# Kernel optimization log

Hardware: AMD Instinct MI355X
Metric: run time of the kernel (lower is better)

## Reference

```python
import math
import jax, jax.numpy as jnp
import numpy as np

N_KV = 8
GROUP = 4
HEAD_DIM = 128
BATCH = 512
CACHE = 2048
CONTEXT = 4096
NEG_INF = -10000.0


def setup_inputs() -> dict:
    key = jax.random.key(0)
    k = jax.random.split(key, 6)
    queries = jax.random.normal(k[0], (N_KV * GROUP, BATCH, HEAD_DIM), jnp.float32)
    keys = jax.random.normal(k[1], (N_KV, BATCH, HEAD_DIM), jnp.float32)
    key_t_caches = jax.random.normal(k[2], (N_KV, HEAD_DIM, CACHE), jnp.float32)
    values = jax.random.normal(k[3], (N_KV, BATCH, HEAD_DIM), jnp.float32)
    value_caches = jax.random.normal(k[4], (N_KV, CACHE, HEAD_DIM), jnp.float32)
    # causal bias: token b (global position CACHE+b) may attend to positions <= CACHE+b;
    # padded tail [CACHE+BATCH, CONTEXT) is always masked with NEG_INF
    pos = jnp.arange(CONTEXT)[None, :]                       # [1, CONTEXT]
    limit = (CACHE + jnp.arange(BATCH))[:, None]             # [BATCH, 1]
    attn_bias = jnp.where(pos <= limit, 0.0, NEG_INF).astype(jnp.float32)
    kq_scale = jnp.asarray([1.0 / math.sqrt(HEAD_DIM)], jnp.float32)
    return {
        "queries": queries,
        "keys": keys,
        "key_t_caches": key_t_caches,
        "values": values,
        "value_caches": value_caches,
        "attn_bias": attn_bias,
        "kq_scale": kq_scale,
    }


def reference(queries, keys, key_t_caches, values, value_caches, attn_bias, kq_scale):
    n_kv, B, D = keys.shape
    n_heads = queries.shape[0]
    group = n_heads // n_kv
    cache = key_t_caches.shape[-1]
    context = attn_bias.shape[-1]
    pad = context - cache - B

    scaled_keys = keys * kq_scale                            # [kv, B, D]
    scaled_values = jnp.maximum(values, NEG_INF)             # [kv, B, D]

    # pad new keys/values to fill context, then prepend cache (matches torch pad+cat)
    padded_kt = jnp.pad(scaled_keys.transpose(0, 2, 1), ((0, 0), (0, 0), (0, pad)))
    all_keys_t = jnp.concatenate([key_t_caches, padded_kt], axis=-1)   # [kv, D, context]
    padded_v = jnp.pad(scaled_values, ((0, 0), (0, pad), (0, 0)))
    all_values = jnp.concatenate([value_caches, padded_v], axis=1)     # [kv, context, D]

    q = queries.reshape(n_kv, group, B, D)                   # group-major per kv head
    scores = jnp.einsum('kgbd,kdc->kgbc', q, all_keys_t) + attn_bias   # [kv, g, B, context]
    probs = jax.nn.softmax(scores, axis=-1)
    out = jnp.einsum('kgbc,kcd->kgbd', probs, all_values)    # [kv, g, B, D]
    head_outs = out.reshape(n_heads, B, D)
    return head_outs, scaled_keys, scaled_values
```

## Files before the change

### kernel.cpp

```cpp
#include <hip/hip_runtime.h>
#include <hip/hip_bf16.h>

#define NKV 8
#define NHEADS 32
#define HDIM 128
#define BATCH 512
#define CACHE 2048
#define CTX_TOT 2560
#define CT 64
#define KPITCH 136
#define VPITCH 72
#define PPITCH 72
#define NEG_BIG (-1e30f)

typedef __attribute__((ext_vector_type(8))) _Float16 half8;
typedef __attribute__((ext_vector_type(4))) float floatx4;


__global__ void kprep(const float* __restrict__ ktc, _Float16* __restrict__ Kh) {
    __shared__ float tile[32][33];
    int kv = blockIdx.z, c0 = blockIdx.x * 32, d0 = blockIdx.y * 32;
    int x = threadIdx.x, y = threadIdx.y;
    const float* src = ktc + ((size_t)kv * HDIM + d0) * CACHE + c0;
#pragma unroll
    for (int i = 0; i < 4; i++)
        tile[y + 8 * i][x] = src[(size_t)(y + 8 * i) * CACHE + x];
    __syncthreads();
    _Float16* dst = Kh + ((size_t)kv * CTX_TOT + c0) * HDIM + d0;
#pragma unroll
    for (int i = 0; i < 4; i++)
        dst[(size_t)(y + 8 * i) * HDIM + x] = (_Float16)tile[x][y + 8 * i];
}

__global__ void vprep(const float* __restrict__ vc, _Float16* __restrict__ Vth) {
    __shared__ float tile[32][33];
    int kv = blockIdx.z, c0 = blockIdx.x * 32, d0 = blockIdx.y * 32;
    int x = threadIdx.x, y = threadIdx.y;
    const float* src = vc + ((size_t)kv * CACHE + c0) * HDIM + d0;
#pragma unroll
    for (int i = 0; i < 4; i++)
        tile[y + 8 * i][x] = src[(size_t)(y + 8 * i) * HDIM + x];
    __syncthreads();
    _Float16* dst = Vth + ((size_t)kv * HDIM + d0) * CTX_TOT + c0;
#pragma unroll
    for (int i = 0; i < 4; i++)
        dst[(size_t)(y + 8 * i) * CTX_TOT + x] = (_Float16)tile[x][y + 8 * i];
}

__global__ void knew(const float* __restrict__ keys, const float* __restrict__ kq,
                     float* __restrict__ outk, _Float16* __restrict__ Kh) {
    int i = blockIdx.x * 256 + threadIdx.x;
    float s = kq[0];
    float v = keys[i] * s;
    outk[i] = v;
    int kv = i >> 16;
    int rem = i & 0xFFFF;
    Kh[((size_t)kv * CTX_TOT + CACHE) * HDIM + rem] = (_Float16)v;
}

__global__ void vnew(const float* __restrict__ values, float* __restrict__ outv,
                     _Float16* __restrict__ Vth) {
    __shared__ float tile[32][33];
    int kv = blockIdx.z, b0 = blockIdx.x * 32, d0 = blockIdx.y * 32;
    int x = threadIdx.x, y = threadIdx.y;
    const float* src = values + ((size_t)kv * BATCH + b0) * HDIM + d0;
    float* dst32 = outv + ((size_t)kv * BATCH + b0) * HDIM + d0;
#pragma unroll
    for (int i = 0; i < 4; i++) {
        float v = fmaxf(src[(size_t)(y + 8 * i) * HDIM + x], -10000.0f);
        tile[y + 8 * i][x] = v;
        dst32[(size_t)(y + 8 * i) * HDIM + x] = v;
    }
    __syncthreads();
    _Float16* dst = Vth + ((size_t)kv * HDIM + d0) * CTX_TOT + CACHE + b0;
#pragma unroll
    for (int i = 0; i < 4; i++)
        dst[(size_t)(y + 8 * i) * CTX_TOT + x] = (_Float16)tile[x][y + 8 * i];
}

__global__ __launch_bounds__(256) void attn_main(const float* __restrict__ q_g,
                                                 const _Float16* __restrict__ Kh,
                                                 const _Float16* __restrict__ Vth,
                                                 float* __restrict__ out) {
    __shared__ _Float16 Klds[CT * KPITCH];
    __shared__ _Float16 Vlds[HDIM * VPITCH];
    __shared__ _Float16 Plds[4][16 * PPITCH];

    const int h = blockIdx.x & 31;
    const int qb = blockIdx.x >> 5;
    const int kv = h >> 2;
    const int t = threadIdx.x;
    const int wave = t >> 6;
    const int lane = t & 63;
    const int l15 = lane & 15, quad = lane >> 4;

    const float LOG2E = 1.44269504088896340736f;
    const int qrow0 = qb * 64 + wave * 16;
    const float* qp = q_g + ((size_t)h * BATCH + qrow0 + l15) * HDIM + quad * 8;
    half8 qfrag[4];
#pragma unroll
    for (int kb = 0; kb < 4; kb++) {
        const float* p = qp + kb * 32;
        float4 a = *(const float4*)p;
        float4 b = *(const float4*)(p + 4);
        qfrag[kb][0] = (_Float16)(a.x * LOG2E); qfrag[kb][1] = (_Float16)(a.y * LOG2E);
        qfrag[kb][2] = (_Float16)(a.z * LOG2E); qfrag[kb][3] = (_Float16)(a.w * LOG2E);
        qfrag[kb][4] = (_Float16)(b.x * LOG2E); qfrag[kb][5] = (_Float16)(b.y * LOG2E);
        qfrag[kb][6] = (_Float16)(b.z * LOG2E); qfrag[kb][7] = (_Float16)(b.w * LOG2E);
    }

    floatx4 O[8];
#pragma unroll
    for (int nb = 0; nb < 8; nb++) O[nb] = (floatx4){0.f, 0.f, 0.f, 0.f};
    float m_r[4], l_r[4];
#pragma unroll
    for (int r = 0; r < 4; r++) { m_r[r] = NEG_BIG; l_r[r] = 0.f; }

    const int lim_wave = CACHE + qrow0 + 15;
    const int nT = 33 + qb;

    for (int tt = 0; tt < nT; tt++) {
        const int c0 = tt * CT;
        __syncthreads();
#pragma unroll
        for (int i = 0; i < 4; i++) {
            int ch = t + 256 * i;
            int row = ch >> 4, j = ch & 15;
            uint4 v = *(const uint4*)(Kh + ((size_t)kv * CTX_TOT + c0 + row) * HDIM + j * 8);
            *(uint4*)(&Klds[row * KPITCH + j * 8]) = v;
        }
#pragma unroll
        for (int i = 0; i < 4; i++) {
            int ch = t + 256 * i;
            int row = ch >> 3, j = ch & 7;
            uint4 v = *(const uint4*)(Vth + ((size_t)kv * HDIM + row) * CTX_TOT + c0 + j * 8);
            *(uint4*)(&Vlds[row * VPITCH + j * 8]) = v;
        }
        __syncthreads();

        if (c0 <= lim_wave) {
            floatx4 S[4];
#pragma unroll
            for (int cs = 0; cs < 4; cs++) {
                floatx4 acc = (floatx4){0.f, 0.f, 0.f, 0.f};
                int crow = cs * 16 + l15;
#pragma unroll
                for (int kb = 0; kb < 4; kb++) {
                    half8 kf = *(const half8*)(&Klds[crow * KPITCH + kb * 32 + quad * 8]);
                    acc = __builtin_amdgcn_mfma_f32_16x16x32_f16(qfrag[kb], kf, acc, 0, 0, 0);
                }
                S[cs] = acc;
            }
            if (c0 + CT > CACHE + qb * 64) {
#pragma unroll
                for (int cs = 0; cs < 4; cs++)
#pragma unroll
                    for (int r = 0; r < 4; r++) {
                        int c = c0 + cs * 16 + l15;
                        int brow = qrow0 + quad * 4 + r;
                        if (c > CACHE + brow) S[cs][r] = NEG_BIG;
                    }
            }
            float tmax[4];
#pragma unroll
            for (int r = 0; r < 4; r++)
                tmax[r] = fmaxf(fmaxf(S[0][r], S[1][r]), fmaxf(S[2][r], S[3][r]));
#pragma unroll
            for (int off = 8; off >= 1; off >>= 1)
#pragma unroll
                for (int r = 0; r < 4; r++)
                    tmax[r] = fmaxf(tmax[r], __shfl_xor(tmax[r], off, 64));
            float alpha[4];
#pragma unroll
            for (int r = 0; r < 4; r++) {
                float mn = fmaxf(m_r[r], tmax[r]);
                alpha[r] = __builtin_amdgcn_exp2f(m_r[r] - mn);
                m_r[r] = mn;
                l_r[r] *= alpha[r];
            }
#pragma unroll
            for (int nb = 0; nb < 8; nb++)
#pragma unroll
                for (int r = 0; r < 4; r++) O[nb][r] *= alpha[r];
#pragma unroll
            for (int cs = 0; cs < 4; cs++)
#pragma unroll
                for (int r = 0; r < 4; r++) {
                    float p = __builtin_amdgcn_exp2f(S[cs][r] - m_r[r]);
                    l_r[r] += p;
                    Plds[wave][(quad * 4 + r) * PPITCH + cs * 16 + l15] = (_Float16)p;
                }
#pragma unroll
            for (int kb2 = 0; kb2 < 2; kb2++) {
                half8 pf = *(const half8*)(&Plds[wave][l15 * PPITCH + kb2 * 32 + quad * 8]);
#pragma unroll
                for (int nb = 0; nb < 8; nb++) {
                    half8 vf = *(const half8*)(&Vlds[(nb * 16 + l15) * VPITCH + kb2 * 32 + quad * 8]);
                    O[nb] = __builtin_amdgcn_mfma_f32_16x16x32_f16(pf, vf, O[nb], 0, 0, 0);
                }
            }
        }
    }

#pragma unroll
    for (int off = 8; off >= 1; off >>= 1)
#pragma unroll
        for (int r = 0; r < 4; r++) l_r[r] += __shfl_xor(l_r[r], off, 64);
    float inv[4];
#pragma unroll
    for (int r = 0; r < 4; r++) inv[r] = 1.0f / l_r[r];
#pragma unroll
    for (int nb = 0; nb < 8; nb++)
#pragma unroll
        for (int r = 0; r < 4; r++) {
            int brow = qrow0 + quad * 4 + r;
            out[((size_t)h * BATCH + brow) * HDIM + nb * 16 + l15] = O[nb][r] * inv[r];
        }
}

extern "C" void kernel_launch(void* const* d_in, const int* in_sizes, int n_in,
                              void* d_out, int out_size, void* d_ws, size_t ws_size,
                              hipStream_t stream) {
    const float* queries = (const float*)d_in[0];
    const float* keys    = (const float*)d_in[1];
    const float* ktc     = (const float*)d_in[2];
    const float* values  = (const float*)d_in[3];
    const float* vcache  = (const float*)d_in[4];
    const float* kq      = (const float*)d_in[6];

    float* out     = (float*)d_out;
    float* out_sk  = out + (size_t)NHEADS * BATCH * HDIM;
    float* out_sv  = out_sk + (size_t)NKV * BATCH * HDIM;

    _Float16* Kh  = (_Float16*)d_ws;
    _Float16* Vth = Kh + (size_t)NKV * CTX_TOT * HDIM;

    kprep<<<dim3(64, 4, 8), dim3(32, 8), 0, stream>>>(ktc, Kh);
    vprep<<<dim3(64, 4, 8), dim3(32, 8), 0, stream>>>(vcache, Vth);
    knew<<<dim3(2048), dim3(256), 0, stream>>>(keys, kq, out_sk, Kh);
    vnew<<<dim3(16, 4, 8), dim3(32, 8), 0, stream>>>(values, out_sv, Vth);
    attn_main<<<dim3(256), dim3(256), 0, stream>>>(queries, Kh, Vth, out);
}
```

Before: 177.9 us.

## Split attention context across blocks with merge kernel and fuse prep kernels

Merges the four preprocessing kernels into one launch that dispatches on block index. It also splits each head/query-block's context loop four ways (interleaved tiles) across a second grid dimension, so there are 1024 blocks instead of 256. Each split writes unnormalized partial outputs plus its running max and sum, and a new merge kernel combines them with exp2 reweighting. This is meant to fix the low occupancy of only 256 blocks on a large GPU and cut launch overhead. The cost is extra workspace traffic for the partial results and one more kernel launch.

```diff
diff --git a/kernel.cpp b/kernel.cpp
--- a/kernel.cpp
+++ b/kernel.cpp
@@ -8,6 +8,7 @@
 #define CACHE 2048
 #define CTX_TOT 2560
 #define CT 64
+#define SPLITS 4
 #define KPITCH 136
 #define VPITCH 72
 #define PPITCH 72
@@ -16,78 +17,83 @@
 typedef __attribute__((ext_vector_type(8))) _Float16 half8;
 typedef __attribute__((ext_vector_type(4))) float floatx4;
 
-
-__global__ void kprep(const float* __restrict__ ktc, _Float16* __restrict__ Kh) {
+__global__ __launch_bounds__(256) void prep(const float* __restrict__ ktc,
+                                            const float* __restrict__ vc,
+                                            const float* __restrict__ keys,
+                                            const float* __restrict__ values,
+                                            const float* __restrict__ kq,
+                                            float* __restrict__ outk,
+                                            float* __restrict__ outv,
+                                            _Float16* __restrict__ Kh,
+                                            _Float16* __restrict__ Vth) {
     __shared__ float tile[32][33];
-    int kv = blockIdx.z, c0 = blockIdx.x * 32, d0 = blockIdx.y * 32;
-    int x = threadIdx.x, y = threadIdx.y;
-    const float* src = ktc + ((size_t)kv * HDIM + d0) * CACHE + c0;
-#pragma unroll
-    for (int i = 0; i < 4; i++)
-        tile[y + 8 * i][x] = src[(size_t)(y + 8 * i) * CACHE + x];
-    __syncthreads();
-    _Float16* dst = Kh + ((size_t)kv * CTX_TOT + c0) * HDIM + d0;
-#pragma unroll
-    for (int i = 0; i < 4; i++)
-        dst[(size_t)(y + 8 * i) * HDIM + x] = (_Float16)tile[x][y + 8 * i];
-}
-
-__global__ void vprep(const float* __restrict__ vc, _Float16* __restrict__ Vth) {
-    __shared__ float tile[32][33];
-    int kv = blockIdx.z, c0 = blockIdx.x * 32, d0 = blockIdx.y * 32;
-    int x = threadIdx.x, y = threadIdx.y;
-    const float* src = vc + ((size_t)kv * CACHE + c0) * HDIM + d0;
-#pragma unroll
-    for (int i = 0; i < 4; i++)
-        tile[y + 8 * i][x] = src[(size_t)(y + 8 * i) * HDIM + x];
-    __syncthreads();
-    _Float16* dst = Vth + ((size_t)kv * HDIM + d0) * CTX_TOT + c0;
-#pragma unroll
-    for (int i = 0; i < 4; i++)
-        dst[(size_t)(y + 8 * i) * CTX_TOT + x] = (_Float16)tile[x][y + 8 * i];
-}
-
-__global__ void knew(const float* __restrict__ keys, const float* __restrict__ kq,
-                     float* __restrict__ outk, _Float16* __restrict__ Kh) {
-    int i = blockIdx.x * 256 + threadIdx.x;
-    float s = kq[0];
-    float v = keys[i] * s;
-    outk[i] = v;
-    int kv = i >> 16;
-    int rem = i & 0xFFFF;
-    Kh[((size_t)kv * CTX_TOT + CACHE) * HDIM + rem] = (_Float16)v;
-}
-
-__global__ void vnew(const float* __restrict__ values, float* __restrict__ outv,
-                     _Float16* __restrict__ Vth) {
-    __shared__ float tile[32][33];
-    int kv = blockIdx.z, b0 = blockIdx.x * 32, d0 = blockIdx.y * 32;
-    int x = threadIdx.x, y = threadIdx.y;
-    const float* src = values + ((size_t)kv * BATCH + b0) * HDIM + d0;
-    float* dst32 = outv + ((size_t)kv * BATCH + b0) * HDIM + d0;
-#pragma unroll
-    for (int i = 0; i < 4; i++) {
-        float v = fmaxf(src[(size_t)(y + 8 * i) * HDIM + x], -10000.0f);
-        tile[y + 8 * i][x] = v;
-        dst32[(size_t)(y + 8 * i) * HDIM + x] = v;
-    }
-    __syncthreads();
-    _Float16* dst = Vth + ((size_t)kv * HDIM + d0) * CTX_TOT + CACHE + b0;
-#pragma unroll
-    for (int i = 0; i < 4; i++)
-        dst[(size_t)(y + 8 * i) * CTX_TOT + x] = (_Float16)tile[x][y + 8 * i];
-}
-
-__global__ __launch_bounds__(256) void attn_main(const float* __restrict__ q_g,
-                                                 const _Float16* __restrict__ Kh,
-                                                 const _Float16* __restrict__ Vth,
-                                                 float* __restrict__ out) {
+    const int bid = blockIdx.x;
+    const int t = threadIdx.x;
+    const int x = t & 31, y = t >> 5;
+
+    if (bid < 2048) {
+        int l = bid;
+        int c0 = (l & 63) * 32, d0 = ((l >> 6) & 3) * 32, kv = l >> 8;
+        const float* src = ktc + ((size_t)kv * HDIM + d0) * CACHE + c0;
+#pragma unroll
+        for (int i = 0; i < 4; i++)
+            tile[y + 8 * i][x] = src[(size_t)(y + 8 * i) * CACHE + x];
+        __syncthreads();
+        _Float16* dst = Kh + ((size_t)kv * CTX_TOT + c0) * HDIM + d0;
+#pragma unroll
+        for (int i = 0; i < 4; i++)
+            dst[(size_t)(y + 8 * i) * HDIM + x] = (_Float16)tile[x][y + 8 * i];
+    } else if (bid < 4096) {
+        int l = bid - 2048;
+        int c0 = (l & 63) * 32, d0 = ((l >> 6) & 3) * 32, kv = l >> 8;
+        const float* src = vc + ((size_t)kv * CACHE + c0) * HDIM + d0;
+#pragma unroll
+        for (int i = 0; i < 4; i++)
+            tile[y + 8 * i][x] = src[(size_t)(y + 8 * i) * HDIM + x];
+        __syncthreads();
+        _Float16* dst = Vth + ((size_t)kv * HDIM + d0) * CTX_TOT + c0;
+#pragma unroll
+        for (int i = 0; i < 4; i++)
+            dst[(size_t)(y + 8 * i) * CTX_TOT + x] = (_Float16)tile[x][y + 8 * i];
+    } else if (bid < 6144) {
+        int i = (bid - 4096) * 256 + t;
+        float s = kq[0];
+        float v = keys[i] * s;
+        outk[i] = v;
+        int kv = i >> 16;
+        int rem = i & 0xFFFF;
+        Kh[((size_t)kv * CTX_TOT + CACHE) * HDIM + rem] = (_Float16)v;
+    } else {
+        int l = bid - 6144;
+        int b0 = (l & 15) * 32, d0 = ((l >> 4) & 3) * 32, kv = l >> 6;
+        const float* src = values + ((size_t)kv * BATCH + b0) * HDIM + d0;
+        float* dst32 = outv + ((size_t)kv * BATCH + b0) * HDIM + d0;
+#pragma unroll
+        for (int i = 0; i < 4; i++) {
+            float v = fmaxf(src[(size_t)(y + 8 * i) * HDIM + x], -10000.0f);
+            tile[y + 8 * i][x] = v;
+            dst32[(size_t)(y + 8 * i) * HDIM + x] = v;
+        }
+        __syncthreads();
+        _Float16* dst = Vth + ((size_t)kv * HDIM + d0) * CTX_TOT + CACHE + b0;
+#pragma unroll
+        for (int i = 0; i < 4; i++)
+            dst[(size_t)(y + 8 * i) * CTX_TOT + x] = (_Float16)tile[x][y + 8 * i];
+    }
+}
+
+__global__ __launch_bounds__(256) void attn_split(const float* __restrict__ q_g,
+                                                  const _Float16* __restrict__ Kh,
+                                                  const _Float16* __restrict__ Vth,
+                                                  float* __restrict__ Opart,
+                                                  float* __restrict__ MLpart) {
     __shared__ _Float16 Klds[CT * KPITCH];
     __shared__ _Float16 Vlds[HDIM * VPITCH];
     __shared__ _Float16 Plds[4][16 * PPITCH];
 
     const int h = blockIdx.x & 31;
     const int qb = blockIdx.x >> 5;
+    const int s = blockIdx.y;
     const int kv = h >> 2;
     const int t = threadIdx.x;
     const int wave = t >> 6;
@@ -119,7 +125,7 @@
     const int lim_wave = CACHE + qrow0 + 15;
     const int nT = 33 + qb;
 
-    for (int tt = 0; tt < nT; tt++) {
+    for (int tt = s; tt < nT; tt += SPLITS) {
         const int c0 = tt * CT;
         __syncthreads();
 #pragma unroll
@@ -206,16 +212,53 @@
     for (int off = 8; off >= 1; off >>= 1)
 #pragma unroll
         for (int r = 0; r < 4; r++) l_r[r] += __shfl_xor(l_r[r], off, 64);
-    float inv[4];
-#pragma unroll
-    for (int r = 0; r < 4; r++) inv[r] = 1.0f / l_r[r];
+
+    const size_t rowbase = (size_t)s * NHEADS * BATCH + (size_t)h * BATCH;
 #pragma unroll
     for (int nb = 0; nb < 8; nb++)
 #pragma unroll
         for (int r = 0; r < 4; r++) {
             int brow = qrow0 + quad * 4 + r;
-            out[((size_t)h * BATCH + brow) * HDIM + nb * 16 + l15] = O[nb][r] * inv[r];
-        }
+            Opart[(rowbase + brow) * HDIM + nb * 16 + l15] = O[nb][r];
+        }
+    if (l15 == 0) {
+#pragma unroll
+        for (int r = 0; r < 4; r++) {
+            int brow = qrow0 + quad * 4 + r;
+            MLpart[(rowbase + brow) * 2 + 0] = m_r[r];
+            MLpart[(rowbase + brow) * 2 + 1] = l_r[r];
+        }
+    }
+}
+
+__global__ __launch_bounds__(256) void attn_merge(const float* __restrict__ Opart,
+                                                  const float* __restrict__ MLpart,
+                                                  float* __restrict__ out) {
+    const int t = threadIdx.x;
+    const int row = blockIdx.x * 2 + (t >> 7);
+    const int d = t & 127;
+    const size_t stride = (size_t)NHEADS * BATCH;
+
+    float m0 = MLpart[((size_t)0 * stride + row) * 2];
+    float m1 = MLpart[((size_t)1 * stride + row) * 2];
+    float m2 = MLpart[((size_t)2 * stride + row) * 2];
+    float m3 = MLpart[((size_t)3 * stride + row) * 2];
+    float l0 = MLpart[((size_t)0 * stride + row) * 2 + 1];
+    float l1 = MLpart[((size_t)1 * stride + row) * 2 + 1];
+    float l2 = MLpart[((size_t)2 * stride + row) * 2 + 1];
+    float l3 = MLpart[((size_t)3 * stride + row) * 2 + 1];
+    float mm = fmaxf(fmaxf(m0, m1), fmaxf(m2, m3));
+    float w0 = __builtin_amdgcn_exp2f(m0 - mm);
+    float w1 = __builtin_amdgcn_exp2f(m1 - mm);
+    float w2 = __builtin_amdgcn_exp2f(m2 - mm);
+    float w3 = __builtin_amdgcn_exp2f(m3 - mm);
+    float denom = w0 * l0 + w1 * l1 + w2 * l2 + w3 * l3;
+
+    float acc = w0 * Opart[((size_t)0 * stride + row) * HDIM + d]
+              + w1 * Opart[((size_t)1 * stride + row) * HDIM + d]
+              + w2 * Opart[((size_t)2 * stride + row) * HDIM + d]
+              + w3 * Opart[((size_t)3 * stride + row) * HDIM + d];
+    out[(size_t)row * HDIM + d] = acc / denom;
 }
 
 extern "C" void kernel_launch(void* const* d_in, const int* in_sizes, int n_in,
@@ -232,12 +275,13 @@
     float* out_sk  = out + (size_t)NHEADS * BATCH * HDIM;
     float* out_sv  = out_sk + (size_t)NKV * BATCH * HDIM;
 
-    _Float16* Kh  = (_Float16*)d_ws;
-    _Float16* Vth = Kh + (size_t)NKV * CTX_TOT * HDIM;
-
-    kprep<<<dim3(64, 4, 8), dim3(32, 8), 0, stream>>>(ktc, Kh);
-    vprep<<<dim3(64, 4, 8), dim3(32, 8), 0, stream>>>(vcache, Vth);
-    knew<<<dim3(2048), dim3(256), 0, stream>>>(keys, kq, out_sk, Kh);
-    vnew<<<dim3(16, 4, 8), dim3(32, 8), 0, stream>>>(values, out_sv, Vth);
-    attn_main<<<dim3(256), dim3(256), 0, stream>>>(queries, Kh, Vth, out);
-}
+    _Float16* Kh   = (_Float16*)d_ws;
+    _Float16* Vth  = Kh + (size_t)NKV * CTX_TOT * HDIM;
+    float*    Opart = (float*)(Vth + (size_t)NKV * HDIM * CTX_TOT);
+    float*    MLpart = Opart + (size_t)SPLITS * NHEADS * BATCH * HDIM;
+
+    prep<<<dim3(6656), dim3(256), 0, stream>>>(ktc, vcache, keys, values, kq,
+                                               out_sk, out_sv, Kh, Vth);
+    attn_split<<<dim3(256, SPLITS), dim3(256), 0, stream>>>(queries, Kh, Vth, Opart, MLpart);
+    attn_merge<<<dim3(8192), dim3(256), 0, stream>>>(Opart, MLpart, out);
+}
```

Result: faster. 156.5 us (-12.0%).
